# Kernel optimization log

Hardware: AMD Instinct MI355X
Metric: run time of the kernel (lower is better)

The kernel has to match this reference:

```python
import jax, jax.numpy as jnp
import numpy as np

B, T = 2, 512
E, NH, HD, V, P, L, KER, BLOCK = 768, 12, 64, 256, 4, 4, 16, 512
SCALE = HD ** -0.5


def _ln(x, g, b, eps=1e-5):
    m = jnp.mean(x, -1, keepdims=True)
    v = jnp.mean((x - m) ** 2, -1, keepdims=True)
    return (x - m) * jax.lax.rsqrt(v + eps) * g + b


def _rope_tables(n):
    inv = 1.0 / (10000.0 ** (jnp.arange(0, HD, 2, dtype=jnp.float32) / HD))
    f = jnp.arange(n, dtype=jnp.float32)[:, None] * inv[None, :]
    return jnp.cos(f), jnp.sin(f)


def _rope(x, cos, sin):
    # rotate over last two dims (positions, HD); split-half RoPE as in source
    h = x.shape[-1] // 2
    x1, x2 = x[..., :h], x[..., h:]
    return jnp.concatenate([x1 * cos - x2 * sin, x1 * sin + x2 * cos], axis=-1)


def _patch_attn(x, qkv_w, S):
    # x: [B,T,E]; sliding-window patch attention, step=1
    Bb, Tt, _ = x.shape
    q, k, v = jnp.split(x @ qkv_w, 3, axis=-1)
    heads = lambda t: t.reshape(Bb, Tt, NH, HD).transpose(0, 2, 1, 3)  # [B,NH,T,HD]
    q, k, v = heads(q), heads(k), heads(v)
    cos, sin = _rope_tables(Tt)
    q = _rope(q, cos, sin)
    k = _rope(k, cos, sin)
    # prefix: full causal attention over first S tokens
    sc = jnp.einsum('bnqh,bnkh->bnqk', q[:, :, :S], k[:, :, :S]) * SCALE
    mask = jnp.tril(jnp.ones((S, S), dtype=bool))
    sc = jnp.where(mask, sc, jnp.float32(-jnp.inf))
    out = jnp.einsum('bnqk,bnkh->bnqh', jax.nn.softmax(sc, axis=-1), v[:, :, :S])
    if Tt > S:
        # query t (t>=S) attends keys [t-S+1, t] (mask_sliding is all-ones for step=1)
        idx = jnp.arange(Tt - S)[:, None] + 1 + jnp.arange(S)[None, :]  # [T-S,S]
        kw = k[:, :, idx]  # [B,NH,T-S,S,HD]
        vw = v[:, :, idx]
        qs = q[:, :, S:]   # [B,NH,T-S,HD]
        sw = jnp.einsum('bnth,bntsh->bnts', qs, kw) * SCALE
        ow = jnp.einsum('bnts,bntsh->bnth', jax.nn.softmax(sw, axis=-1), vw)
        out = jnp.concatenate([out, ow], axis=2)
    return out.transpose(0, 2, 1, 3).reshape(Bb, Tt, NH * HD)


def _sa_block(x, ln0g, ln0b, ln1g, ln1b, qkv_w, proj_w, proj_b, w1, b1, w2, b2):
    # x: [B,T,P,V]; full (unmasked) attention over the P prediction slots
    Bb, Tt, Pp, _ = x.shape
    h = _ln(x, ln0g, ln0b)
    q, k, v = jnp.split(h @ qkv_w, 3, axis=-1)
    heads = lambda t: t.reshape(Bb, Tt, Pp, NH, HD).transpose(0, 1, 3, 2, 4)  # [B,T,NH,P,HD]
    q, k, v = heads(q), heads(k), heads(v)
    cos, sin = _rope_tables(Pp)
    q = _rope(q, cos, sin)
    k = _rope(k, cos, sin)
    sc = jnp.einsum('btnph,btnqh->btnpq', q, k) * SCALE
    o = jnp.einsum('btnpq,btnqh->btnph', jax.nn.softmax(sc, axis=-1), v)
    o = o.transpose(0, 1, 3, 2, 4).reshape(Bb, Tt, Pp, NH * HD)
    x = x + (o @ proj_w + proj_b)
    h2 = _ln(x, ln1g, ln1b)
    ff = jax.nn.gelu(h2 @ w1 + b1, approximate=False) @ w2 + b2
    return x + ff


def _forward(tokens, emb, blk_ln0_g, blk_ln0_b, blk_ln1_g, blk_ln1_b, blk_qkv_w,
             blk_ff_w1, blk_ff_b1, blk_ff_w2, blk_ff_b2, fin_ln_g, fin_ln_b,
             head_w, head_b, sa_ln0_g, sa_ln0_b, sa_ln1_g, sa_ln1_b, sa_qkv_w,
             sa_proj_w, sa_proj_b, sa_ff_w1, sa_ff_b1, sa_ff_w2, sa_ff_b2):
    x0 = emb[tokens]  # [B,T,E]
    x = x0
    for i in range(L):
        S = min(KER * 2 ** i, BLOCK)
        h = _ln(x, blk_ln0_g[i], blk_ln0_b[i])
        x = x + _patch_attn(h, blk_qkv_w[i], S)
        h2 = _ln(x, blk_ln1_g[i], blk_ln1_b[i])
        x = x + (jax.nn.gelu(h2 @ blk_ff_w1[i] + blk_ff_b1[i], approximate=False)
                 @ blk_ff_w2[i] + blk_ff_b2[i])
    x = x0 + x  # Golu: x = token_embedding(x); x = x + blocks(x)
    x = _ln(x, fin_ln_g, fin_ln_b)
    logits = (x @ head_w + head_b).reshape(B, T, P, V)
    logits = _sa_block(logits, sa_ln0_g, sa_ln0_b, sa_ln1_g, sa_ln1_b, sa_qkv_w,
                       sa_proj_w, sa_proj_b, sa_ff_w1, sa_ff_b1, sa_ff_w2, sa_ff_b2)
    return logits[:, :, 0, :]  # [B,T,V] (y is None path)


def setup_inputs() -> dict:
    key = jax.random.key(0)
    ks = jax.random.split(key, 12)
    w = lambda k, sh: jax.random.normal(k, sh, dtype=jnp.float32) * 0.02
    return {
        'tokens': jax.random.randint(ks[0], (B, T), 0, V),
        'emb': w(ks[1], (V, E)),
        'blk_ln0_g': jnp.ones((L, E), jnp.float32),
        'blk_ln0_b': jnp.zeros((L, E), jnp.float32),
        'blk_ln1_g': jnp.ones((L, E), jnp.float32),
        'blk_ln1_b': jnp.zeros((L, E), jnp.float32),
        'blk_qkv_w': w(ks[2], (L, E, 3 * E)),
        'blk_ff_w1': w(ks[3], (L, E, 4 * E)),
        'blk_ff_b1': jnp.zeros((L, 4 * E), jnp.float32),
        'blk_ff_w2': w(ks[4], (L, 4 * E, E)),
        'blk_ff_b2': jnp.zeros((L, E), jnp.float32),
        'fin_ln_g': jnp.ones((E,), jnp.float32),
        'fin_ln_b': jnp.zeros((E,), jnp.float32),
        'head_w': w(ks[5], (E, V * P)),
        'head_b': jnp.zeros((V * P,), jnp.float32),
        'sa_ln0_g': jnp.ones((V,), jnp.float32),
        'sa_ln0_b': jnp.zeros((V,), jnp.float32),
        'sa_ln1_g': jnp.ones((V,), jnp.float32),
        'sa_ln1_b': jnp.zeros((V,), jnp.float32),
        'sa_qkv_w': w(ks[6], (V, 3 * E)),
        'sa_proj_w': w(ks[7], (E, V)),
        'sa_proj_b': jnp.zeros((V,), jnp.float32),
        'sa_ff_w1': w(ks[8], (V, 4 * V)),
        'sa_ff_b1': jnp.zeros((4 * V,), jnp.float32),
        'sa_ff_w2': w(ks[9], (4 * V, V)),
        'sa_ff_b2': jnp.zeros((V,), jnp.float32),
    }


def reference(tokens, emb, blk_ln0_g, blk_ln0_b, blk_ln1_g, blk_ln1_b, blk_qkv_w,
              blk_ff_w1, blk_ff_b1, blk_ff_w2, blk_ff_b2, fin_ln_g, fin_ln_b,
              head_w, head_b, sa_ln0_g, sa_ln0_b, sa_ln1_g, sa_ln1_b, sa_qkv_w,
              sa_proj_w, sa_proj_b, sa_ff_w1, sa_ff_b1, sa_ff_w2, sa_ff_b2):
    return _forward(tokens, emb, blk_ln0_g, blk_ln0_b, blk_ln1_g, blk_ln1_b,
                    blk_qkv_w, blk_ff_w1, blk_ff_b1, blk_ff_w2, blk_ff_b2,
                    fin_ln_g, fin_ln_b, head_w, head_b, sa_ln0_g, sa_ln0_b,
                    sa_ln1_g, sa_ln1_b, sa_qkv_w, sa_proj_w, sa_proj_b,
                    sa_ff_w1, sa_ff_b1, sa_ff_w2, sa_ff_b2)
```

## Files before the change

### kernel.cpp

```cpp
#include <hip/hip_runtime.h>
#include <hip/hip_bf16.h>
#include <cstdint>
#include <cstddef>

#define BB    2
#define TSEQ  512
#define EDIM  768
#define NHEAD 12
#define HDIM  64
#define VDIM  256
#define PDIM  4
#define NROW  (BB*TSEQ)
#define NROW2 (BB*TSEQ*PDIM)

typedef __attribute__((ext_vector_type(8))) short short8;
typedef __attribute__((ext_vector_type(4))) float floatx4;

__device__ __forceinline__ float gelu_f(float v){
    return 0.5f * v * (1.0f + erff(v * 0.70710678118654752f));
}

__device__ __forceinline__ float b2f(short s){
    unsigned u = ((unsigned)(unsigned short)s) << 16;
    float f; __builtin_memcpy(&f, &u, 4); return f;
}

__device__ __forceinline__ void gload16(const void* g, void* l){
    __builtin_amdgcn_global_load_lds((const __attribute__((address_space(1))) void*)g,
                                     (__attribute__((address_space(3))) void*)l, 16, 0, 0);
}

struct WD { const float* in; __hip_bfloat16* out; int K; int N; int ntiles; };

__global__ __launch_bounds__(256) void wconv_multi(WD d0, WD d1, WD d2, WD d3, WD d4)
{
    int id = blockIdx.x;
    WD w = d0;
    if(id >= w.ntiles){ id -= w.ntiles; w = d1;
        if(id >= w.ntiles){ id -= w.ntiles; w = d2;
            if(id >= w.ntiles){ id -= w.ntiles; w = d3;
                if(id >= w.ntiles){ id -= w.ntiles; w = d4; } } } }
    if(!w.in) return;
    const int tx = w.N / 32;
    const int n0 = (id % tx) * 32, k0 = (id / tx) * 32;
    __shared__ float t[32][33];
    const int c = threadIdx.x & 31, r0 = threadIdx.x >> 5;
    #pragma unroll
    for(int r = r0; r < 32; r += 8)
        t[r][c] = w.in[(size_t)(k0 + r) * w.N + n0 + c];
    __syncthreads();
    #pragma unroll
    for(int r = r0; r < 32; r += 8)
        w.out[(size_t)(n0 + r) * w.K + k0 + c] = __float2bfloat16(t[c][r]);
}

template<int ACT, int RESID, int OUTBF16, int ROPESA>
__global__ __launch_bounds__(256) void gemm128(
    const short* __restrict__ A, const short* __restrict__ Bt,
    const float* __restrict__ bias, const float* __restrict__ resid,
    void* __restrict__ Cout, const float* __restrict__ rc, const float* __restrict__ rs,
    int M, int N, int K)
{
    alignas(16) __shared__ short As[128*32];
    alignas(16) __shared__ short Bs[128*32];
    const int tid  = threadIdx.x;
    const int lane = tid & 63;
    const int wave = tid >> 6;
    const int bm = blockIdx.y * 128, bn = blockIdx.x * 128;
    const int wm = (wave >> 1) * 64, wn = (wave & 1) * 64;
    const int quad = lane >> 4, l16 = lane & 15;

    floatx4 acc[4][4];
    #pragma unroll
    for(int i = 0; i < 4; i++)
        #pragma unroll
        for(int j = 0; j < 4; j++)
            acc[i][j] = floatx4{0.f, 0.f, 0.f, 0.f};

    const int r  = tid >> 2;
    const int c8 = (tid & 3) * 8;
    const int ldsoff = (tid & 192) * 16;

    for(int k0 = 0; k0 < K; k0 += 32){
        gload16(A  + (size_t)(bm + r     ) * K + k0 + c8, (char*)As + ldsoff);
        gload16(A  + (size_t)(bm + r + 64) * K + k0 + c8, (char*)As + 4096 + ldsoff);
        gload16(Bt + (size_t)(bn + r     ) * K + k0 + c8, (char*)Bs + ldsoff);
        gload16(Bt + (size_t)(bn + r + 64) * K + k0 + c8, (char*)Bs + 4096 + ldsoff);
        __syncthreads();
        short8 af[4], bfr[4];
        #pragma unroll
        for(int i = 0; i < 4; i++){
            af[i]  = *(const short8*)&As[(wm + i*16 + l16)*32 + quad*8];
            bfr[i] = *(const short8*)&Bs[(wn + i*16 + l16)*32 + quad*8];
        }
        #pragma unroll
        for(int i = 0; i < 4; i++)
            #pragma unroll
            for(int j = 0; j < 4; j++)
                acc[i][j] = __builtin_amdgcn_mfma_f32_16x16x32_bf16(af[i], bfr[j], acc[i][j], 0, 0, 0);
        __syncthreads();
    }

    float* Cf = (float*)Cout;
    __hip_bfloat16* Cb = (__hip_bfloat16*)Cout;

    if(ROPESA){
        const int hb = bn + wn;
        const int region = hb / 768;
        #pragma unroll
        for(int i = 0; i < 4; i++){
            #pragma unroll
            for(int rr = 0; rr < 4; rr++){
                int row = bm + wm + i*16 + quad*4 + rr;
                float a0 = acc[i][0][rr], a1 = acc[i][1][rr];
                float a2 = acc[i][2][rr], a3 = acc[i][3][rr];
                size_t rowb = (size_t)row * N + hb;
                if(region == 2){
                    Cb[rowb + l16]      = __float2bfloat16(a0);
                    Cb[rowb + 16 + l16] = __float2bfloat16(a1);
                    Cb[rowb + 32 + l16] = __float2bfloat16(a2);
                    Cb[rowb + 48 + l16] = __float2bfloat16(a3);
                }else{
                    int p = row & 3;
                    float c0 = rc[p*32 + l16],      s0 = rs[p*32 + l16];
                    float c1 = rc[p*32 + 16 + l16], s1 = rs[p*32 + 16 + l16];
                    Cb[rowb + l16]      = __float2bfloat16(a0*c0 - a2*s0);
                    Cb[rowb + 16 + l16] = __float2bfloat16(a1*c1 - a3*s1);
                    Cb[rowb + 32 + l16] = __float2bfloat16(a0*s0 + a2*c0);
                    Cb[rowb + 48 + l16] = __float2bfloat16(a1*s1 + a3*c1);
                }
            }
        }
        return;
    }

    #pragma unroll
    for(int i = 0; i < 4; i++){
        int row0 = bm + wm + i*16 + quad*4;
        #pragma unroll
        for(int j = 0; j < 4; j++){
            int col = bn + wn + j*16 + l16;
            float bv = bias ? bias[col] : 0.f;
            #pragma unroll
            for(int rr = 0; rr < 4; rr++){
                float v = acc[i][j][rr] + bv;
                if(ACT) v = gelu_f(v);
                if(RESID) v += resid[(size_t)(row0 + rr) * N + col];
                if(OUTBF16) Cb[(size_t)(row0 + rr) * N + col] = __float2bfloat16(v);
                else        Cf[(size_t)(row0 + rr) * N + col] = v;
            }
        }
    }
}

template<int EPI>
__global__ __launch_bounds__(256) void gemm64x128(
    const short* __restrict__ A, const short* __restrict__ Bt,
    const float* __restrict__ bias, __hip_bfloat16* __restrict__ Cout,
    __hip_bfloat16* __restrict__ qrb, __hip_bfloat16* __restrict__ krb,
    __hip_bfloat16* __restrict__ vvb,
    const float* __restrict__ rc, const float* __restrict__ rs,
    int M, int N, int K)
{
    alignas(16) __shared__ short As[64*32];
    alignas(16) __shared__ short Bs[128*32];
    const int tid  = threadIdx.x;
    const int lane = tid & 63;
    const int wave = tid >> 6;
    const int bm = blockIdx.y * 64, bn = blockIdx.x * 128;
    const int wm = (wave >> 1) * 32, wn = (wave & 1) * 64;
    const int quad = lane >> 4, l16 = lane & 15;

    floatx4 acc[2][4];
    #pragma unroll
    for(int i = 0; i < 2; i++)
        #pragma unroll
        for(int j = 0; j < 4; j++)
            acc[i][j] = floatx4{0.f, 0.f, 0.f, 0.f};

    const int r  = tid >> 2;
    const int c8 = (tid & 3) * 8;
    const int ldsoff = (tid & 192) * 16;

    for(int k0 = 0; k0 < K; k0 += 32){
        gload16(A  + (size_t)(bm + r     ) * K + k0 + c8, (char*)As + ldsoff);
        gload16(Bt + (size_t)(bn + r     ) * K + k0 + c8, (char*)Bs + ldsoff);
        gload16(Bt + (size_t)(bn + r + 64) * K + k0 + c8, (char*)Bs + 4096 + ldsoff);
        __syncthreads();
        short8 af[2], bfr[4];
        #pragma unroll
        for(int i = 0; i < 2; i++)
            af[i]  = *(const short8*)&As[(wm + i*16 + l16)*32 + quad*8];
        #pragma unroll
        for(int j = 0; j < 4; j++)
            bfr[j] = *(const short8*)&Bs[(wn + j*16 + l16)*32 + quad*8];
        #pragma unroll
        for(int i = 0; i < 2; i++)
            #pragma unroll
            for(int j = 0; j < 4; j++)
                acc[i][j] = __builtin_amdgcn_mfma_f32_16x16x32_bf16(af[i], bfr[j], acc[i][j], 0, 0, 0);
        __syncthreads();
    }

    if(EPI == 2){
        const int hb = bn + wn;
        const int region = hb / 768;
        const int h = (hb % 768) >> 6;
        #pragma unroll
        for(int i = 0; i < 2; i++){
            #pragma unroll
            for(int rr = 0; rr < 4; rr++){
                int row = bm + wm + i*16 + quad*4 + rr;
                int t = row & (TSEQ-1), b = row >> 9;
                float a0 = acc[i][0][rr], a1 = acc[i][1][rr];
                float a2 = acc[i][2][rr], a3 = acc[i][3][rr];
                size_t dbase = ((size_t)(b*NHEAD + h)*TSEQ + t)*HDIM;
                if(region == 2){
                    vvb[dbase + l16]      = __float2bfloat16(a0);
                    vvb[dbase + 16 + l16] = __float2bfloat16(a1);
                    vvb[dbase + 32 + l16] = __float2bfloat16(a2);
                    vvb[dbase + 48 + l16] = __float2bfloat16(a3);
                }else{
                    float c0 = rc[t*32 + l16],      s0 = rs[t*32 + l16];
                    float c1 = rc[t*32 + 16 + l16], s1 = rs[t*32 + 16 + l16];
                    __hip_bfloat16* dst = (region == 0) ? qrb : krb;
                    dst[dbase + l16]      = __float2bfloat16(a0*c0 - a2*s0);
                    dst[dbase + 16 + l16] = __float2bfloat16(a1*c1 - a3*s1);
                    dst[dbase + 32 + l16] = __float2bfloat16(a0*s0 + a2*c0);
                    dst[dbase + 48 + l16] = __float2bfloat16(a1*s1 + a3*c1);
                }
            }
        }
        return;
    }

    #pragma unroll
    for(int i = 0; i < 2; i++){
        int row0 = bm + wm + i*16 + quad*4;
        #pragma unroll
        for(int j = 0; j < 4; j++){
            int col = bn + wn + j*16 + l16;
            float bv = bias ? bias[col] : 0.f;
            #pragma unroll
            for(int rr = 0; rr < 4; rr++){
                float v = acc[i][j][rr] + bv;
                if(EPI == 1) v = gelu_f(v);
                Cout[(size_t)(row0 + rr) * N + col] = __float2bfloat16(v);
            }
        }
    }
}

template<int ACT, int RESID, int OUTBF16>
__global__ __launch_bounds__(256) void gemm64t(
    const short* __restrict__ A, const short* __restrict__ Bt,
    const float* __restrict__ bias, const float* __restrict__ resid,
    void* __restrict__ Cout, int M, int N, int K)
{
    alignas(16) __shared__ short As[64*32];
    alignas(16) __shared__ short Bs[64*32];
    const int tid  = threadIdx.x;
    const int lane = tid & 63;
    const int wave = tid >> 6;
    const int bm = blockIdx.y * 64, bn = blockIdx.x * 64;
    const int wm = (wave >> 1) * 32, wn = (wave & 1) * 32;
    const int quad = lane >> 4, l16 = lane & 15;

    floatx4 acc[2][2];
    #pragma unroll
    for(int i = 0; i < 2; i++)
        #pragma unroll
        for(int j = 0; j < 2; j++)
            acc[i][j] = floatx4{0.f, 0.f, 0.f, 0.f};

    const int r  = tid >> 2;
    const int c8 = (tid & 3) * 8;
    const int ldsoff = (tid & 192) * 16;

    for(int k0 = 0; k0 < K; k0 += 32){
        gload16(A  + (size_t)(bm + r) * K + k0 + c8, (char*)As + ldsoff);
        gload16(Bt + (size_t)(bn + r) * K + k0 + c8, (char*)Bs + ldsoff);
        __syncthreads();
        short8 af[2], bfr[2];
        #pragma unroll
        for(int i = 0; i < 2; i++){
            af[i]  = *(const short8*)&As[(wm + i*16 + l16)*32 + quad*8];
            bfr[i] = *(const short8*)&Bs[(wn + i*16 + l16)*32 + quad*8];
        }
        #pragma unroll
        for(int i = 0; i < 2; i++)
            #pragma unroll
            for(int j = 0; j < 2; j++)
                acc[i][j] = __builtin_amdgcn_mfma_f32_16x16x32_bf16(af[i], bfr[j], acc[i][j], 0, 0, 0);
        __syncthreads();
    }

    float* Cf = (float*)Cout;
    __hip_bfloat16* Cb = (__hip_bfloat16*)Cout;
    #pragma unroll
    for(int i = 0; i < 2; i++){
        int row0 = bm + wm + i*16 + quad*4;
        #pragma unroll
        for(int j = 0; j < 2; j++){
            int col = bn + wn + j*16 + l16;
            float bv = bias ? bias[col] : 0.f;
            #pragma unroll
            for(int rr = 0; rr < 4; rr++){
                float v = acc[i][j][rr] + bv;
                if(ACT) v = gelu_f(v);
                if(RESID) v += resid[(size_t)(row0 + rr) * N + col];
                if(OUTBF16) Cb[(size_t)(row0 + rr) * N + col] = __float2bfloat16(v);
                else        Cf[(size_t)(row0 + rr) * N + col] = v;
            }
        }
    }
}

__global__ __launch_bounds__(256) void ln_kernel(
    const float* __restrict__ in, const float* __restrict__ in2,
    const float* __restrict__ g, const float* __restrict__ bta,
    __hip_bfloat16* __restrict__ out, int D)
{
    const int row = blockIdx.x;
    const float* xr  = in + (size_t)row * D;
    const float* x2r = in2 ? in2 + (size_t)row * D : nullptr;
    const int tid = threadIdx.x;
    const int nper = D / 256;
    float vals[3];
    float sum = 0.f, sq = 0.f;
    for(int i = 0; i < nper; i++){
        int d = tid + i*256;
        float v = xr[d];
        if(x2r) v += x2r[d];
        vals[i] = v; sum += v; sq += v*v;
    }
    #pragma unroll
    for(int off = 32; off > 0; off >>= 1){
        sum += __shfl_xor(sum, off, 64);
        sq  += __shfl_xor(sq,  off, 64);
    }
    __shared__ float ssum[4], ssq[4];
    __shared__ float smean, srstd;
    int wid = tid >> 6;
    if((tid & 63) == 0){ ssum[wid] = sum; ssq[wid] = sq; }
    __syncthreads();
    if(tid == 0){
        float S = 0.f, Q = 0.f;
        for(int w = 0; w < 4; w++){ S += ssum[w]; Q += ssq[w]; }
        float m = S / D;
        float var = Q / D - m*m;
        smean = m;
        srstd = rsqrtf(fmaxf(var, 0.f) + 1e-5f);
    }
    __syncthreads();
    float m = smean, rs2 = srstd;
    for(int i = 0; i < nper; i++){
        int d = tid + i*256;
        out[(size_t)row*D + d] = __float2bfloat16((vals[i] - m) * rs2 * g[d] + bta[d]);
    }
}

__global__ __launch_bounds__(192) void embed_kernel(
    const int* __restrict__ tokens, const float* __restrict__ emb,
    float* __restrict__ x0, float* __restrict__ x)
{
    const int row = blockIdx.x;
    const int tok = tokens[row];
    const float4* src = (const float4*)(emb + (size_t)tok * EDIM);
    float4* d0 = (float4*)(x0 + (size_t)row * EDIM);
    float4* d1 = (float4*)(x  + (size_t)row * EDIM);
    for(int i = threadIdx.x; i < EDIM/4; i += blockDim.x){
        float4 v = src[i]; d0[i] = v; d1[i] = v;
    }
}

__global__ __launch_bounds__(256) void rope_kernel(float* __restrict__ rc, float* __restrict__ rs)
{
    int i = blockIdx.x * 256 + threadIdx.x;
    int pos = i >> 5, d = i & 31;
    float inv = powf(10000.0f, -(float)(2*d) / 64.0f);
    float f = (float)pos * inv;
// ... 82 lines not shown
    const int t = blockIdx.x, h = blockIdx.y, b = blockIdx.z;
    const int p = threadIdx.x >> 6, lane = threadIdx.x & 63;
    const int row0 = (b*TSEQ + t) * PDIM;
    const short* base = (const short*)qkv2 + (size_t)row0 * (3*EDIM);
    const int d = lane;
    float q = b2f(base[(size_t)p*(3*EDIM) + h*HDIM + d]);
    float sc[4];
    #pragma unroll
    for(int j = 0; j < 4; j++){
        float kj = b2f(base[(size_t)j*(3*EDIM) + EDIM + h*HDIM + d]);
        float v = q * kj;
        #pragma unroll
        for(int off = 32; off > 0; off >>= 1) v += __shfl_xor(v, off, 64);
        sc[j] = v * 0.125f;
    }
    float m = fmaxf(fmaxf(sc[0], sc[1]), fmaxf(sc[2], sc[3]));
    float e0 = expf(sc[0]-m), e1 = expf(sc[1]-m), e2 = expf(sc[2]-m), e3 = expf(sc[3]-m);
    float idn = 1.f / (e0 + e1 + e2 + e3);
    float ov = (e0 * b2f(base[0*(3*EDIM) + 2*EDIM + h*HDIM + d])
              + e1 * b2f(base[1*(3*EDIM) + 2*EDIM + h*HDIM + d])
              + e2 * b2f(base[2*(3*EDIM) + 2*EDIM + h*HDIM + d])
              + e3 * b2f(base[3*(3*EDIM) + 2*EDIM + h*HDIM + d])) * idn;
    o[(size_t)(row0 + p) * EDIM + h*HDIM + d] = __float2bfloat16(ov);
}

__global__ __launch_bounds__(256) void outcopy(const float* __restrict__ x2, float* __restrict__ out)
{
    int i = blockIdx.x * 256 + threadIdx.x;
    int row = i >> 8, col = i & 255;
    out[i] = x2[(size_t)row * PDIM * VDIM + col];
}

extern "C" void kernel_launch(void* const* d_in, const int* in_sizes, int n_in,
                              void* d_out, int out_size, void* d_ws, size_t ws_size,
                              hipStream_t stream)
{
    const int*   tokens    = (const int*)  d_in[0];
    const float* emb       = (const float*)d_in[1];
    const float* bl0g      = (const float*)d_in[2];
    const float* bl0b      = (const float*)d_in[3];
    const float* bl1g      = (const float*)d_in[4];
    const float* bl1b      = (const float*)d_in[5];
    const float* qkv_w     = (const float*)d_in[6];
    const float* ff_w1     = (const float*)d_in[7];
    const float* ff_b1     = (const float*)d_in[8];
    const float* ff_w2     = (const float*)d_in[9];
    const float* ff_b2     = (const float*)d_in[10];
    const float* fin_g     = (const float*)d_in[11];
    const float* fin_b     = (const float*)d_in[12];
    const float* head_w    = (const float*)d_in[13];
    const float* head_b    = (const float*)d_in[14];
    const float* sa_ln0_g  = (const float*)d_in[15];
    const float* sa_ln0_b  = (const float*)d_in[16];
    const float* sa_ln1_g  = (const float*)d_in[17];
    const float* sa_ln1_b  = (const float*)d_in[18];
    const float* sa_qkv_w  = (const float*)d_in[19];
    const float* sa_proj_w = (const float*)d_in[20];
    const float* sa_proj_b = (const float*)d_in[21];
    const float* sa_ff_w1  = (const float*)d_in[22];
    const float* sa_ff_b1  = (const float*)d_in[23];
    const float* sa_ff_w2  = (const float*)d_in[24];
    const float* sa_ff_b2  = (const float*)d_in[25];
    float* out = (float*)d_out;

    char* base = (char*)d_ws;
    float* logits           = (float*)(base);
    float* ropec            = (float*)(base + 4194304);
    float* ropes            = (float*)(base + 4259840);
    __hip_bfloat16* wqkvT   = (__hip_bfloat16*)(base + 4325376);
    __hip_bfloat16* wff1T   = (__hip_bfloat16*)(base + 7864320);
    __hip_bfloat16* wff2T   = (__hip_bfloat16*)(base + 12582912);
    __hip_bfloat16* wheadT  = (__hip_bfloat16*)(base + 17301504);
    __hip_bfloat16* wsaqkvT = (__hip_bfloat16*)(base + 18874368);
    __hip_bfloat16* wsaprojT= (__hip_bfloat16*)(base + 20054016);
    __hip_bfloat16* wsaff1T = (__hip_bfloat16*)(base + 20447232);
    __hip_bfloat16* wsaff2T = (__hip_bfloat16*)(base + 20971520);
    char* U = base + 21495808;
    float* x0           = (float*)(U);
    float* x            = (float*)(U + 3145728);
    __hip_bfloat16* h   = (__hip_bfloat16*)(U + 6291456);
    __hip_bfloat16* ff1 = (__hip_bfloat16*)(U + 12582912);
    __hip_bfloat16* qrb = (__hip_bfloat16*)(U + 18874368);
    __hip_bfloat16* krb = (__hip_bfloat16*)(U + 20447232);
    __hip_bfloat16* vvb = (__hip_bfloat16*)(U + 22020096);
    __hip_bfloat16* h2    = (__hip_bfloat16*)(U);
    __hip_bfloat16* qkv2  = (__hip_bfloat16*)(U + 2097152);
    __hip_bfloat16* sa_o  = (__hip_bfloat16*)(U + 20971520);
    __hip_bfloat16* sa_f1 = (__hip_bfloat16*)(U + 27262976);

    embed_kernel<<<NROW, 192, 0, stream>>>(tokens, emb, x0, x);
    rope_kernel<<<64, 256, 0, stream>>>(ropec, ropes);
    {
        WD dh  = { head_w,    wheadT,   768,  1024, (1024/32)*( 768/32) };
        WD dq  = { sa_qkv_w,  wsaqkvT,  256,  2304, (2304/32)*( 256/32) };
        WD dp  = { sa_proj_w, wsaprojT, 768,   256, ( 256/32)*( 768/32) };
        WD df1 = { sa_ff_w1,  wsaff1T,  256,  1024, (1024/32)*( 256/32) };
        WD df2 = { sa_ff_w2,  wsaff2T, 1024,   256, ( 256/32)*(1024/32) };
        wconv_multi<<<768+576+192+256+256, 256, 0, stream>>>(dh, dq, dp, df1, df2);
    }

    for(int i = 0; i < 4; i++){
        {
            WD dq  = { qkv_w + (size_t)i*EDIM*3*EDIM, wqkvT, 768, 2304, (2304/32)*(768/32) };
            WD df1 = { ff_w1 + (size_t)i*EDIM*4*EDIM, wff1T, 768, 3072, (3072/32)*(768/32) };
            WD df2 = { ff_w2 + (size_t)i*4*EDIM*EDIM, wff2T, 3072, 768, ( 768/32)*(3072/32)};
            WD dn  = { nullptr, nullptr, 0, 0, 0 };
            wconv_multi<<<1728+2304+2304, 256, 0, stream>>>(dq, df1, df2, dn, dn);
        }
        ln_kernel<<<NROW, 256, 0, stream>>>(x, nullptr, bl0g + i*EDIM, bl0b + i*EDIM, h, EDIM);
        gemm64x128<2><<<dim3(18, 16), 256, 0, stream>>>(
            (const short*)h, (const short*)wqkvT, nullptr, nullptr,
            qrb, krb, vvb, ropec, ropes, NROW, 3*EDIM, EDIM);
        dim3 agrid(TSEQ/4, NHEAD, BB);
        if(i == 0)      patch_attn2<16><<<agrid, 256, 0, stream>>>(qrb, krb, vvb, x);
        else if(i == 1) patch_attn2<32><<<agrid, 256, 0, stream>>>(qrb, krb, vvb, x);
        else if(i == 2) patch_attn2<64><<<agrid, 256, 0, stream>>>(qrb, krb, vvb, x);
        else            patch_attn2<128><<<agrid, 256, 0, stream>>>(qrb, krb, vvb, x);
        ln_kernel<<<NROW, 256, 0, stream>>>(x, nullptr, bl1g + i*EDIM, bl1b + i*EDIM, h, EDIM);
        gemm64x128<1><<<dim3(24, 16), 256, 0, stream>>>(
            (const short*)h, (const short*)wff1T, ff_b1 + (size_t)i*4*EDIM, ff1,
            nullptr, nullptr, nullptr, nullptr, nullptr, NROW, 4*EDIM, EDIM);
        gemm64t<0,1,0><<<dim3(12, 16), 256, 0, stream>>>(
            (const short*)ff1, (const short*)wff2T, ff_b2 + (size_t)i*EDIM, x, x, NROW, EDIM, 4*EDIM);
    }

    ln_kernel<<<NROW, 256, 0, stream>>>(x, x0, fin_g, fin_b, h, EDIM);
    gemm64t<0,0,0><<<dim3(16, 16), 256, 0, stream>>>(
        (const short*)h, (const short*)wheadT, head_b, nullptr, logits, NROW, PDIM*VDIM, EDIM);

    ln_kernel<<<NROW2, 256, 0, stream>>>(logits, nullptr, sa_ln0_g, sa_ln0_b, h2, VDIM);
    gemm128<0,0,1,1><<<dim3(18, 32), 256, 0, stream>>>(
        (const short*)h2, (const short*)wsaqkvT, nullptr, nullptr, qkv2,
        ropec, ropes, NROW2, 3*EDIM, VDIM);
    sa_attn<<<dim3(TSEQ, NHEAD, BB), 256, 0, stream>>>(qkv2, sa_o);
    gemm64t<0,1,0><<<dim3(4, 64), 256, 0, stream>>>(
        (const short*)sa_o, (const short*)wsaprojT, sa_proj_b, logits, logits, NROW2, VDIM, EDIM);
    ln_kernel<<<NROW2, 256, 0, stream>>>(logits, nullptr, sa_ln1_g, sa_ln1_b, h2, VDIM);
    gemm128<1,0,1,0><<<dim3(8, 32), 256, 0, stream>>>(
        (const short*)h2, (const short*)wsaff1T, sa_ff_b1, nullptr, sa_f1,
        nullptr, nullptr, NROW2, 4*VDIM, VDIM);
    gemm64t<0,1,0><<<dim3(4, 64), 256, 0, stream>>>(
        (const short*)sa_f1, (const short*)wsaff2T, sa_ff_b2, logits, logits, NROW2, VDIM, 4*VDIM);

    outcopy<<<(out_size + 255)/256, 256, 0, stream>>>(logits, out);
}
```

Baseline: 736.5 us.

## Fuse LayerNorm into GEMM prologues by folding gamma/beta into weights and bias

Removes the standalone LayerNorm kernels. Gamma is folded into the transposed bf16 weights, and beta@W is precomputed into a bias vector. Each GEMM computes per-row mean and rstd and normalizes its A tile on the fly from fp32. All weight conversions for the four layers are batched into one launch up front, and the final output copy is fused into the last GEMM epilogue. This cuts launches and intermediate bf16 round trips, but each GEMM column block now re-reads fp32 activations for its statistics. The A tile is also loaded synchronously instead of with direct-to-LDS loads.

```diff
diff --git a/kernel.cpp b/kernel.cpp
--- a/kernel.cpp
+++ b/kernel.cpp
@@ -19,28 +19,28 @@
 __device__ __forceinline__ float gelu_f(float v){
     return 0.5f * v * (1.0f + erff(v * 0.70710678118654752f));
 }
-
 __device__ __forceinline__ float b2f(short s){
     unsigned u = ((unsigned)(unsigned short)s) << 16;
     float f; __builtin_memcpy(&f, &u, 4); return f;
 }
-
+__device__ __forceinline__ short f2bs(float v){
+    __hip_bfloat16 h = __float2bfloat16(v);
+    short s; __builtin_memcpy(&s, &h, 2); return s;
+}
 __device__ __forceinline__ void gload16(const void* g, void* l){
     __builtin_amdgcn_global_load_lds((const __attribute__((address_space(1))) void*)g,
                                      (__attribute__((address_space(3))) void*)l, 16, 0, 0);
 }
 
-struct WD { const float* in; __hip_bfloat16* out; int K; int N; int ntiles; };
-
-__global__ __launch_bounds__(256) void wconv_multi(WD d0, WD d1, WD d2, WD d3, WD d4)
+struct WD2 { const float* in; const float* g; __hip_bfloat16* out; int K; int N; int nt; };
+struct WDs { WD2 d[17]; };
+
+__global__ __launch_bounds__(256) void wconv_all(WDs a)
 {
     int id = blockIdx.x;
-    WD w = d0;
-    if(id >= w.ntiles){ id -= w.ntiles; w = d1;
-        if(id >= w.ntiles){ id -= w.ntiles; w = d2;
-            if(id >= w.ntiles){ id -= w.ntiles; w = d3;
-                if(id >= w.ntiles){ id -= w.ntiles; w = d4; } } } }
-    if(!w.in) return;
+    int i = 0;
+    while(i < 16 && id >= a.d[i].nt){ id -= a.d[i].nt; i++; }
+    WD2 w = a.d[i];
     const int tx = w.N / 32;
     const int n0 = (id % tx) * 32, k0 = (id / tx) * 32;
     __shared__ float t[32][33];
@@ -48,31 +48,83 @@
     #pragma unroll
     for(int r = r0; r < 32; r += 8)
         t[r][c] = w.in[(size_t)(k0 + r) * w.N + n0 + c];
+    const float gv = w.g ? w.g[k0 + c] : 1.0f;
     __syncthreads();
     #pragma unroll
     for(int r = r0; r < 32; r += 8)
-        w.out[(size_t)(n0 + r) * w.K + k0 + c] = __float2bfloat16(t[c][r]);
-}
-
-template<int ACT, int RESID, int OUTBF16, int ROPESA>
-__global__ __launch_bounds__(256) void gemm128(
-    const short* __restrict__ A, const short* __restrict__ Bt,
-    const float* __restrict__ bias, const float* __restrict__ resid,
-    void* __restrict__ Cout, const float* __restrict__ rc, const float* __restrict__ rs,
+        w.out[(size_t)(n0 + r) * w.K + k0 + c] = __float2bfloat16(t[c][r] * gv);
+}
+
+struct LB { const float* extb; const float* lnb; const float* w; float* ob; int N; int K; };
+struct LBs { LB d[11]; };
+
+__global__ __launch_bounds__(256) void lnbias(LBs a)
+{
+    int id = blockIdx.x;
+    int i = 0;
+    while(i < 10 && id >= a.d[i].N/256){ id -= a.d[i].N/256; i++; }
+    LB w = a.d[i];
+    const int n = id*256 + threadIdx.x;
+    float acc = w.extb ? w.extb[n] : 0.f;
+    for(int k = 0; k < w.K; k += 4){
+        acc += w.lnb[k+0] * w.w[(size_t)(k+0)*w.N + n];
+        acc += w.lnb[k+1] * w.w[(size_t)(k+1)*w.N + n];
+        acc += w.lnb[k+2] * w.w[(size_t)(k+2)*w.N + n];
+        acc += w.lnb[k+3] * w.w[(size_t)(k+3)*w.N + n];
+    }
+    w.ob[n] = acc;
+}
+
+template<int MT, int EPI, int ADD2>
+__global__ __launch_bounds__(256) void gemmln(
+    const float* __restrict__ A, const float* __restrict__ A2,
+    const short* __restrict__ Bt, const float* __restrict__ biasv,
+    void* __restrict__ Cout,
+    __hip_bfloat16* __restrict__ qrb, __hip_bfloat16* __restrict__ krb,
+    __hip_bfloat16* __restrict__ vvb,
+    const float* __restrict__ rc, const float* __restrict__ rs,
     int M, int N, int K)
 {
-    alignas(16) __shared__ short As[128*32];
+    constexpr int MI = (MT == 64) ? 2 : 4;
+    alignas(16) __shared__ short As[MT*32];
     alignas(16) __shared__ short Bs[128*32];
+    __shared__ float smean[MT], srstd[MT];
+
     const int tid  = threadIdx.x;
     const int lane = tid & 63;
     const int wave = tid >> 6;
-    const int bm = blockIdx.y * 128, bn = blockIdx.x * 128;
-    const int wm = (wave >> 1) * 64, wn = (wave & 1) * 64;
+    const int bm = blockIdx.y * MT, bn = blockIdx.x * 128;
+    const int wm = (wave >> 1) * (MT/2), wn = (wave & 1) * 64;
     const int quad = lane >> 4, l16 = lane & 15;
 
-    floatx4 acc[4][4];
-    #pragma unroll
-    for(int i = 0; i < 4; i++)
+    {
+        int sr, seg, off;
+        if(MT == 64){ sr = tid >> 2; seg = K/4; off = (tid & 3) * seg; }
+        else        { sr = tid >> 1; seg = K/2; off = (tid & 1) * seg; }
+        const float* xr  = A + (size_t)(bm + sr) * K + off;
+        const float* x2r = ADD2 ? A2 + (size_t)(bm + sr) * K + off : nullptr;
+        float s = 0.f, q = 0.f;
+        for(int j = 0; j < seg; j += 4){
+            float4 v = *(const float4*)(xr + j);
+            if(ADD2){ float4 w2 = *(const float4*)(x2r + j);
+                      v.x += w2.x; v.y += w2.y; v.z += w2.z; v.w += w2.w; }
+            s += v.x + v.y + v.z + v.w;
+            q += v.x*v.x + v.y*v.y + v.z*v.z + v.w*v.w;
+        }
+        s += __shfl_xor(s, 1, 64); q += __shfl_xor(q, 1, 64);
+        if(MT == 64){ s += __shfl_xor(s, 2, 64); q += __shfl_xor(q, 2, 64); }
+        const int qt = (MT == 64) ? (tid & 3) : (tid & 1);
+        if(qt == 0){
+            float m = s / K;
+            smean[sr] = m;
+            srstd[sr] = rsqrtf(fmaxf(q / K - m*m, 0.f) + 1e-5f);
+        }
+    }
+    __syncthreads();
+
+    floatx4 acc[MI][4];
+    #pragma unroll
+    for(int i = 0; i < MI; i++)
         #pragma unroll
         for(int j = 0; j < 4; j++)
             acc[i][j] = floatx4{0.f, 0.f, 0.f, 0.f};
@@ -80,21 +132,49 @@
     const int r  = tid >> 2;
     const int c8 = (tid & 3) * 8;
     const int ldsoff = (tid & 192) * 16;
+    const float m0 = smean[r], rs0 = srstd[r];
+    float m1 = 0.f, rs1 = 0.f;
+    if(MT == 128){ m1 = smean[r + 64]; rs1 = srstd[r + 64]; }
 
     for(int k0 = 0; k0 < K; k0 += 32){
-        gload16(A  + (size_t)(bm + r     ) * K + k0 + c8, (char*)As + ldsoff);
-        gload16(A  + (size_t)(bm + r + 64) * K + k0 + c8, (char*)As + 4096 + ldsoff);
         gload16(Bt + (size_t)(bn + r     ) * K + k0 + c8, (char*)Bs + ldsoff);
         gload16(Bt + (size_t)(bn + r + 64) * K + k0 + c8, (char*)Bs + 4096 + ldsoff);
+        {
+            const float* ap = A + (size_t)(bm + r) * K + k0 + c8;
+            float4 v0 = *(const float4*)(ap), v1 = *(const float4*)(ap + 4);
+            if(ADD2){
+                const float* a2p = A2 + (size_t)(bm + r) * K + k0 + c8;
+                float4 w0 = *(const float4*)(a2p), w1 = *(const float4*)(a2p + 4);
+                v0.x += w0.x; v0.y += w0.y; v0.z += w0.z; v0.w += w0.w;
+                v1.x += w1.x; v1.y += w1.y; v1.z += w1.z; v1.w += w1.w;
+            }
+            short8 pk;
+            pk[0] = f2bs((v0.x - m0)*rs0); pk[1] = f2bs((v0.y - m0)*rs0);
+            pk[2] = f2bs((v0.z - m0)*rs0); pk[3] = f2bs((v0.w - m0)*rs0);
+            pk[4] = f2bs((v1.x - m0)*rs0); pk[5] = f2bs((v1.y - m0)*rs0);
+            pk[6] = f2bs((v1.z - m0)*rs0); pk[7] = f2bs((v1.w - m0)*rs0);
+            *(short8*)&As[r*32 + c8] = pk;
+        }
+        if(MT == 128){
+            const float* ap = A + (size_t)(bm + r + 64) * K + k0 + c8;
+            float4 v0 = *(const float4*)(ap), v1 = *(const float4*)(ap + 4);
+            short8 pk;
+            pk[0] = f2bs((v0.x - m1)*rs1); pk[1] = f2bs((v0.y - m1)*rs1);
+            pk[2] = f2bs((v0.z - m1)*rs1); pk[3] = f2bs((v0.w - m1)*rs1);
+            pk[4] = f2bs((v1.x - m1)*rs1); pk[5] = f2bs((v1.y - m1)*rs1);
+            pk[6] = f2bs((v1.z - m1)*rs1); pk[7] = f2bs((v1.w - m1)*rs1);
+            *(short8*)&As[(r + 64)*32 + c8] = pk;
+        }
         __syncthreads();
-        short8 af[4], bfr[4];
-        #pragma unroll
-        for(int i = 0; i < 4; i++){
+        short8 af[MI], bfr[4];
+        #pragma unroll
+        for(int i = 0; i < MI; i++)
             af[i]  = *(const short8*)&As[(wm + i*16 + l16)*32 + quad*8];
-            bfr[i] = *(const short8*)&Bs[(wn + i*16 + l16)*32 + quad*8];
-        }
-        #pragma unroll
-        for(int i = 0; i < 4; i++)
+        #pragma unroll
+        for(int j = 0; j < 4; j++)
+            bfr[j] = *(const short8*)&Bs[(wn + j*16 + l16)*32 + quad*8];
+        #pragma unroll
+        for(int i = 0; i < MI; i++)
             #pragma unroll
             for(int j = 0; j < 4; j++)
                 acc[i][j] = __builtin_amdgcn_mfma_f32_16x16x32_bf16(af[i], bfr[j], acc[i][j], 0, 0, 0);
@@ -104,30 +184,54 @@
     float* Cf = (float*)Cout;
     __hip_bfloat16* Cb = (__hip_bfloat16*)Cout;
 
-    if(ROPESA){
+    if(EPI == 2 || EPI == 3){
         const int hb = bn + wn;
         const int region = hb / 768;
-        #pragma unroll
-        for(int i = 0; i < 4; i++){
+        const int h = (hb % 768) >> 6;
+        float bj0 = biasv ? biasv[hb + l16]      : 0.f;
+        float bj1 = biasv ? biasv[hb + 16 + l16] : 0.f;
+        float bj2 = biasv ? biasv[hb + 32 + l16] : 0.f;
+        float bj3 = biasv ? biasv[hb + 48 + l16] : 0.f;
+        #pragma unroll
+        for(int i = 0; i < MI; i++){
             #pragma unroll
             for(int rr = 0; rr < 4; rr++){
                 int row = bm + wm + i*16 + quad*4 + rr;
-                float a0 = acc[i][0][rr], a1 = acc[i][1][rr];
-                float a2 = acc[i][2][rr], a3 = acc[i][3][rr];
-                size_t rowb = (size_t)row * N + hb;
-                if(region == 2){
-                    Cb[rowb + l16]      = __float2bfloat16(a0);
-                    Cb[rowb + 16 + l16] = __float2bfloat16(a1);
-                    Cb[rowb + 32 + l16] = __float2bfloat16(a2);
-                    Cb[rowb + 48 + l16] = __float2bfloat16(a3);
+                float a0 = acc[i][0][rr] + bj0, a1 = acc[i][1][rr] + bj1;
+                float a2 = acc[i][2][rr] + bj2, a3 = acc[i][3][rr] + bj3;
+                if(EPI == 2){
+                    int t = row & (TSEQ-1), b = row >> 9;
+                    size_t dbase = ((size_t)(b*NHEAD + h)*TSEQ + t)*HDIM;
+                    if(region == 2){
+                        vvb[dbase + l16]      = __float2bfloat16(a0);
+                        vvb[dbase + 16 + l16] = __float2bfloat16(a1);
+                        vvb[dbase + 32 + l16] = __float2bfloat16(a2);
+                        vvb[dbase + 48 + l16] = __float2bfloat16(a3);
+                    }else{
+                        float c0 = rc[t*32 + l16],      s0 = rs[t*32 + l16];
+                        float c1 = rc[t*32 + 16 + l16], s1 = rs[t*32 + 16 + l16];
+                        __hip_bfloat16* dst = (region == 0) ? qrb : krb;
+                        dst[dbase + l16]      = __float2bfloat16(a0*c0 - a2*s0);
+                        dst[dbase + 16 + l16] = __float2bfloat16(a1*c1 - a3*s1);
+                        dst[dbase + 32 + l16] = __float2bfloat16(a0*s0 + a2*c0);
+                        dst[dbase + 48 + l16] = __float2bfloat16(a1*s1 + a3*c1);
+                    }
                 }else{
-                    int p = row & 3;
-                    float c0 = rc[p*32 + l16],      s0 = rs[p*32 + l16];
-                    float c1 = rc[p*32 + 16 + l16], s1 = rs[p*32 + 16 + l16];
-                    Cb[rowb + l16]      = __float2bfloat16(a0*c0 - a2*s0);
-                    Cb[rowb + 16 + l16] = __float2bfloat16(a1*c1 - a3*s1);
-                    Cb[rowb + 32 + l16] = __float2bfloat16(a0*s0 + a2*c0);
-                    Cb[rowb + 48 + l16] = __float2bfloat16(a1*s1 + a3*c1);
+                    size_t rowb = (size_t)row * N + hb;
+                    if(region == 2){
+                        Cb[rowb + l16]      = __float2bfloat16(a0);
+                        Cb[rowb + 16 + l16] = __float2bfloat16(a1);
+                        Cb[rowb + 32 + l16] = __float2bfloat16(a2);
+                        Cb[rowb + 48 + l16] = __float2bfloat16(a3);
+                    }else{
+                        int p = row & 3;
+                        float c0 = rc[p*32 + l16],      s0 = rs[p*32 + l16];
+                        float c1 = rc[p*32 + 16 + l16], s1 = rs[p*32 + 16 + l16];
+                        Cb[rowb + l16]      = __float2bfloat16(a0*c0 - a2*s0);
+                        Cb[rowb + 16 + l16] = __float2bfloat16(a1*c1 - a3*s1);
+                        Cb[rowb + 32 + l16] = __float2bfloat16(a0*s0 + a2*c0);
+                        Cb[rowb + 48 + l16] = __float2bfloat16(a1*s1 + a3*c1);
+                    }
                 }
             }
         }
@@ -135,127 +239,27 @@
     }
 
     #pragma unroll
-    for(int i = 0; i < 4; i++){
+    for(int i = 0; i < MI; i++){
         int row0 = bm + wm + i*16 + quad*4;
         #pragma unroll
         for(int j = 0; j < 4; j++){
             int col = bn + wn + j*16 + l16;
-            float bv = bias ? bias[col] : 0.f;
+            float bv = biasv ? biasv[col] : 0.f;
             #pragma unroll
             for(int rr = 0; rr < 4; rr++){
                 float v = acc[i][j][rr] + bv;
-                if(ACT) v = gelu_f(v);
-                if(RESID) v += resid[(size_t)(row0 + rr) * N + col];
-                if(OUTBF16) Cb[(size_t)(row0 + rr) * N + col] = __float2bfloat16(v);
-                else        Cf[(size_t)(row0 + rr) * N + col] = v;
+                if(EPI == 1){ v = gelu_f(v); Cb[(size_t)(row0 + rr) * N + col] = __float2bfloat16(v); }
+                else        {                Cf[(size_t)(row0 + rr) * N + col] = v; }
             }
         }
     }
 }
 
-template<int EPI>
-__global__ __launch_bounds__(256) void gemm64x128(
-    const short* __restrict__ A, const short* __restrict__ Bt,
-    const float* __restrict__ bias, __hip_bfloat16* __restrict__ Cout,
-    __hip_bfloat16* __restrict__ qrb, __hip_bfloat16* __restrict__ krb,
-    __hip_bfloat16* __restrict__ vvb,
-    const float* __restrict__ rc, const float* __restrict__ rs,
-    int M, int N, int K)
-{
-    alignas(16) __shared__ short As[64*32];
-    alignas(16) __shared__ short Bs[128*32];
-    const int tid  = threadIdx.x;
-    const int lane = tid & 63;
-    const int wave = tid >> 6;
-    const int bm = blockIdx.y * 64, bn = blockIdx.x * 128;
-    const int wm = (wave >> 1) * 32, wn = (wave & 1) * 64;
-    const int quad = lane >> 4, l16 = lane & 15;
-
-    floatx4 acc[2][4];
-    #pragma unroll
-    for(int i = 0; i < 2; i++)
-        #pragma unroll
-        for(int j = 0; j < 4; j++)
-            acc[i][j] = floatx4{0.f, 0.f, 0.f, 0.f};
-
-    const int r  = tid >> 2;
-    const int c8 = (tid & 3) * 8;
-    const int ldsoff = (tid & 192) * 16;
-
-    for(int k0 = 0; k0 < K; k0 += 32){
-        gload16(A  + (size_t)(bm + r     ) * K + k0 + c8, (char*)As + ldsoff);
-        gload16(Bt + (size_t)(bn + r     ) * K + k0 + c8, (char*)Bs + ldsoff);
-        gload16(Bt + (size_t)(bn + r + 64) * K + k0 + c8, (char*)Bs + 4096 + ldsoff);
-        __syncthreads();
-        short8 af[2], bfr[4];
-        #pragma unroll
-        for(int i = 0; i < 2; i++)
-            af[i]  = *(const short8*)&As[(wm + i*16 + l16)*32 + quad*8];
-        #pragma unroll
-        for(int j = 0; j < 4; j++)
-            bfr[j] = *(const short8*)&Bs[(wn + j*16 + l16)*32 + quad*8];
-        #pragma unroll
-        for(int i = 0; i < 2; i++)
-            #pragma unroll
-            for(int j = 0; j < 4; j++)
-                acc[i][j] = __builtin_amdgcn_mfma_f32_16x16x32_bf16(af[i], bfr[j], acc[i][j], 0, 0, 0);
-        __syncthreads();
-    }
-
-    if(EPI == 2){
-        const int hb = bn + wn;
-        const int region = hb / 768;
-        const int h = (hb % 768) >> 6;
-        #pragma unroll
-        for(int i = 0; i < 2; i++){
-            #pragma unroll
-            for(int rr = 0; rr < 4; rr++){
-                int row = bm + wm + i*16 + quad*4 + rr;
-                int t = row & (TSEQ-1), b = row >> 9;
-                float a0 = acc[i][0][rr], a1 = acc[i][1][rr];
-                float a2 = acc[i][2][rr], a3 = acc[i][3][rr];
-                size_t dbase = ((size_t)(b*NHEAD + h)*TSEQ + t)*HDIM;
-                if(region == 2){
-                    vvb[dbase + l16]      = __float2bfloat16(a0);
-                    vvb[dbase + 16 + l16] = __float2bfloat16(a1);
-                    vvb[dbase + 32 + l16] = __float2bfloat16(a2);
-                    vvb[dbase + 48 + l16] = __float2bfloat16(a3);
-                }else{
-                    float c0 = rc[t*32 + l16],      s0 = rs[t*32 + l16];
-                    float c1 = rc[t*32 + 16 + l16], s1 = rs[t*32 + 16 + l16];
-                    __hip_bfloat16* dst = (region == 0) ? qrb : krb;
-                    dst[dbase + l16]      = __float2bfloat16(a0*c0 - a2*s0);
-                    dst[dbase + 16 + l16] = __float2bfloat16(a1*c1 - a3*s1);
-                    dst[dbase + 32 + l16] = __float2bfloat16(a0*s0 + a2*c0);
-                    dst[dbase + 48 + l16] = __float2bfloat16(a1*s1 + a3*c1);
-                }
-            }
-        }
-        return;
-    }
-
-    #pragma unroll
-    for(int i = 0; i < 2; i++){
-        int row0 = bm + wm + i*16 + quad*4;
-        #pragma unroll
-        for(int j = 0; j < 4; j++){
-            int col = bn + wn + j*16 + l16;
-            float bv = bias ? bias[col] : 0.f;
-            #pragma unroll
-            for(int rr = 0; rr < 4; rr++){
-                float v = acc[i][j][rr] + bv;
-                if(EPI == 1) v = gelu_f(v);
-                Cout[(size_t)(row0 + rr) * N + col] = __float2bfloat16(v);
-            }
-        }
-    }
-}
-
-template<int ACT, int RESID, int OUTBF16>
+template<int OUTC>
 __global__ __launch_bounds__(256) void gemm64t(
     const short* __restrict__ A, const short* __restrict__ Bt,
     const float* __restrict__ bias, const float* __restrict__ resid,
-    void* __restrict__ Cout, int M, int N, int K)
+    float* __restrict__ Cf, float* __restrict__ outp, int M, int N, int K)
 {
     alignas(16) __shared__ short As[64*32];
     alignas(16) __shared__ short Bs[64*32];
@@ -295,8 +299,6 @@
         __syncthreads();
     }
 
-    float* Cf = (float*)Cout;
-    __hip_bfloat16* Cb = (__hip_bfloat16*)Cout;
     #pragma unroll
     for(int i = 0; i < 2; i++){
         int row0 = bm + wm + i*16 + quad*4;
@@ -306,57 +308,13 @@
             float bv = bias ? bias[col] : 0.f;
             #pragma unroll
             for(int rr = 0; rr < 4; rr++){
-                float v = acc[i][j][rr] + bv;
-                if(ACT) v = gelu_f(v);
-                if(RESID) v += resid[(size_t)(row0 + rr) * N + col];
-                if(OUTBF16) Cb[(size_t)(row0 + rr) * N + col] = __float2bfloat16(v);
-                else        Cf[(size_t)(row0 + rr) * N + col] = v;
+                int row = row0 + rr;
+                float v = acc[i][j][rr] + bv + resid[(size_t)row * N + col];
+                Cf[(size_t)row * N + col] = v;
+                if(OUTC && (row & 3) == 0)
+                    outp[(size_t)(row >> 2) * N + col] = v;
             }
         }
-    }
-}
-
-__global__ __launch_bounds__(256) void ln_kernel(
-    const float* __restrict__ in, const float* __restrict__ in2,
-    const float* __restrict__ g, const float* __restrict__ bta,
-    __hip_bfloat16* __restrict__ out, int D)
-{
-    const int row = blockIdx.x;
-    const float* xr  = in + (size_t)row * D;
-    const float* x2r = in2 ? in2 + (size_t)row * D : nullptr;
-    const int tid = threadIdx.x;
-    const int nper = D / 256;
-    float vals[3];
-    float sum = 0.f, sq = 0.f;
-    for(int i = 0; i < nper; i++){
-        int d = tid + i*256;
-        float v = xr[d];
-        if(x2r) v += x2r[d];
-        vals[i] = v; sum += v; sq += v*v;
-    }
-    #pragma unroll
-    for(int off = 32; off > 0; off >>= 1){
-        sum += __shfl_xor(sum, off, 64);
-        sq  += __shfl_xor(sq,  off, 64);
-    }
-    __shared__ float ssum[4], ssq[4];
-    __shared__ float smean, srstd;
-    int wid = tid >> 6;
-    if((tid & 63) == 0){ ssum[wid] = sum; ssq[wid] = sq; }
-    __syncthreads();
-    if(tid == 0){
-        float S = 0.f, Q = 0.f;
-        for(int w = 0; w < 4; w++){ S += ssum[w]; Q += ssq[w]; }
-        float m = S / D;
-        float var = Q / D - m*m;
-        smean = m;
-        srstd = rsqrtf(fmaxf(var, 0.f) + 1e-5f);
-    }
-    __syncthreads();
-    float m = smean, rs2 = srstd;
-    for(int i = 0; i < nper; i++){
-        int d = tid + i*256;
-        out[(size_t)row*D + d] = __float2bfloat16((vals[i] - m) * rs2 * g[d] + bta[d]);
     }
 }
 
@@ -485,13 +443,6 @@
               + e2 * b2f(base[2*(3*EDIM) + 2*EDIM + h*HDIM + d])
               + e3 * b2f(base[3*(3*EDIM) + 2*EDIM + h*HDIM + d])) * idn;
     o[(size_t)(row0 + p) * EDIM + h*HDIM + d] = __float2bfloat16(ov);
-}
-
-__global__ __launch_bounds__(256) void outcopy(const float* __restrict__ x2, float* __restrict__ out)
-{
-    int i = blockIdx.x * 256 + threadIdx.x;
-    int row = i >> 8, col = i & 255;
-    out[i] = x2[(size_t)row * PDIM * VDIM + col];
 }
 
 extern "C" void kernel_launch(void* const* d_in, const int* in_sizes, int n_in,
@@ -526,84 +477,104 @@
     const float* sa_ff_b2  = (const float*)d_in[25];
     float* out = (float*)d_out;
 
-    char* base = (char*)d_ws;
-    float* logits           = (float*)(base);
-    float* ropec            = (float*)(base + 4194304);
-    float* ropes            = (float*)(base + 4259840);
-    __hip_bfloat16* wqkvT   = (__hip_bfloat16*)(base + 4325376);
-    __hip_bfloat16* wff1T   = (__hip_bfloat16*)(base + 7864320);
-    __hip_bfloat16* wff2T   = (__hip_bfloat16*)(base + 12582912);
-    __hip_bfloat16* wheadT  = (__hip_bfloat16*)(base + 17301504);
-    __hip_bfloat16* wsaqkvT = (__hip_bfloat16*)(base + 18874368);
-    __hip_bfloat16* wsaprojT= (__hip_bfloat16*)(base + 20054016);
-    __hip_bfloat16* wsaff1T = (__hip_bfloat16*)(base + 20447232);
-    __hip_bfloat16* wsaff2T = (__hip_bfloat16*)(base + 20971520);
-    char* U = base + 21495808;
+    char* p = (char*)d_ws;
+    auto alloc = [&](size_t bytes){ char* q = p; p += (bytes + 255) & ~(size_t)255; return q; };
+
+    float* logits = (float*)alloc((size_t)NROW2*VDIM*4);
+    float* ropec  = (float*)alloc(512*32*4);
+    float* ropes  = (float*)alloc(512*32*4);
+    float* qkvb[4];  for(int i=0;i<4;i++) qkvb[i]  = (float*)alloc(2304*4);
+    float* ff1b[4];  for(int i=0;i<4;i++) ff1b[i]  = (float*)alloc(3072*4);
+    float* headb  = (float*)alloc(1024*4);
+    float* saqkvb = (float*)alloc(2304*4);
+    float* saff1b = (float*)alloc(1024*4);
+    __hip_bfloat16* wqkvT[4]; for(int i=0;i<4;i++) wqkvT[i] = (__hip_bfloat16*)alloc((size_t)768*2304*2);
+    __hip_bfloat16* wff1T[4]; for(int i=0;i<4;i++) wff1T[i] = (__hip_bfloat16*)alloc((size_t)768*3072*2);
+    __hip_bfloat16* wff2T[4]; for(int i=0;i<4;i++) wff2T[i] = (__hip_bfloat16*)alloc((size_t)3072*768*2);
+    __hip_bfloat16* wheadT   = (__hip_bfloat16*)alloc((size_t)768*1024*2);
+    __hip_bfloat16* wsaqkvT  = (__hip_bfloat16*)alloc((size_t)256*2304*2);
+    __hip_bfloat16* wsaprojT = (__hip_bfloat16*)alloc((size_t)768*256*2);
+    __hip_bfloat16* wsaff1T  = (__hip_bfloat16*)alloc((size_t)256*1024*2);
+    __hip_bfloat16* wsaff2T  = (__hip_bfloat16*)alloc((size_t)1024*256*2);
+    char* U = p;
     float* x0           = (float*)(U);
     float* x            = (float*)(U + 3145728);
-    __hip_bfloat16* h   = (__hip_bfloat16*)(U + 6291456);
-    __hip_bfloat16* ff1 = (__hip_bfloat16*)(U + 12582912);
-    __hip_bfloat16* qrb = (__hip_bfloat16*)(U + 18874368);
-    __hip_bfloat16* krb = (__hip_bfloat16*)(U + 20447232);
-    __hip_bfloat16* vvb = (__hip_bfloat16*)(U + 22020096);
-    __hip_bfloat16* h2    = (__hip_bfloat16*)(U);
-    __hip_bfloat16* qkv2  = (__hip_bfloat16*)(U + 2097152);
-    __hip_bfloat16* sa_o  = (__hip_bfloat16*)(U + 20971520);
-    __hip_bfloat16* sa_f1 = (__hip_bfloat16*)(U + 27262976);
+    __hip_bfloat16* ff1 = (__hip_bfloat16*)(U + 6291456);
+    __hip_bfloat16* qrb = (__hip_bfloat16*)(U + 12582912);
+    __hip_bfloat16* krb = (__hip_bfloat16*)(U + 14155776);
+    __hip_bfloat16* vvb = (__hip_bfloat16*)(U + 15728640);
+    __hip_bfloat16* qkv2  = (__hip_bfloat16*)(U);
+    __hip_bfloat16* sa_o  = (__hip_bfloat16*)(U + 18874368);
+    __hip_bfloat16* sa_f1 = (__hip_bfloat16*)(U + 25165824);
 
     embed_kernel<<<NROW, 192, 0, stream>>>(tokens, emb, x0, x);
     rope_kernel<<<64, 256, 0, stream>>>(ropec, ropes);
     {
-        WD dh  = { head_w,    wheadT,   768,  1024, (1024/32)*( 768/32) };
-        WD dq  = { sa_qkv_w,  wsaqkvT,  256,  2304, (2304/32)*( 256/32) };
-        WD dp  = { sa_proj_w, wsaprojT, 768,   256, ( 256/32)*( 768/32) };
-        WD df1 = { sa_ff_w1,  wsaff1T,  256,  1024, (1024/32)*( 256/32) };
-        WD df2 = { sa_ff_w2,  wsaff2T, 1024,   256, ( 256/32)*(1024/32) };
-        wconv_multi<<<768+576+192+256+256, 256, 0, stream>>>(dh, dq, dp, df1, df2);
+        WDs wds; int tot = 0, n = 0;
+        auto add = [&](const float* in, const float* g, __hip_bfloat16* o2, int K, int N){
+            wds.d[n++] = WD2{in, g, o2, K, N, (N/32)*(K/32)};
+            tot += (N/32)*(K/32);
+        };
+        for(int i=0;i<4;i++){
+            add(qkv_w + (size_t)i*768*2304, bl0g + i*768, wqkvT[i], 768, 2304);
+            add(ff_w1 + (size_t)i*768*3072, bl1g + i*768, wff1T[i], 768, 3072);
+            add(ff_w2 + (size_t)i*3072*768, nullptr,      wff2T[i], 3072, 768);
+        }
+        add(head_w,    fin_g,    wheadT,   768, 1024);
+        add(sa_qkv_w,  sa_ln0_g, wsaqkvT,  256, 2304);
+        add(sa_proj_w, nullptr,  wsaprojT, 768, 256);
+        add(sa_ff_w1,  sa_ln1_g, wsaff1T,  256, 1024);
+        add(sa_ff_w2,  nullptr,  wsaff2T, 1024, 256);
+        wconv_all<<<tot, 256, 0, stream>>>(wds);
+    }
+    {
+        LBs lbs; int tot = 0, n = 0;
+        auto add = [&](const float* extb, const float* lnb, const float* w, float* ob, int N, int K){
+            lbs.d[n++] = LB{extb, lnb, w, ob, N, K};
+            tot += N/256;
+        };
+        for(int i=0;i<4;i++){
+            add(nullptr,          bl0b + i*768, qkv_w + (size_t)i*768*2304, qkvb[i], 2304, 768);
+            add(ff_b1 + i*3072,   bl1b + i*768, ff_w1 + (size_t)i*768*3072, ff1b[i], 3072, 768);
+        }
+        add(head_b,   fin_b,    head_w,   headb,  1024, 768);
+        add(nullptr,  sa_ln0_b, sa_qkv_w, saqkvb, 2304, 256);
+        add(sa_ff_b1, sa_ln1_b, sa_ff_w1, saff1b, 1024, 256);
+        lnbias<<<tot, 256, 0, stream>>>(lbs);
     }
 
     for(int i = 0; i < 4; i++){
-        {
-            WD dq  = { qkv_w + (size_t)i*EDIM*3*EDIM, wqkvT, 768, 2304, (2304/32)*(768/32) };
-            WD df1 = { ff_w1 + (size_t)i*EDIM*4*EDIM, wff1T, 768, 3072, (3072/32)*(768/32) };
-            WD df2 = { ff_w2 + (size_t)i*4*EDIM*EDIM, wff2T, 3072, 768, ( 768/32)*(3072/32)};
-            WD dn  = { nullptr, nullptr, 0, 0, 0 };
-            wconv_multi<<<1728+2304+2304, 256, 0, stream>>>(dq, df1, df2, dn, dn);
-        }
-        ln_kernel<<<NROW, 256, 0, stream>>>(x, nullptr, bl0g + i*EDIM, bl0b + i*EDIM, h, EDIM);
-        gemm64x128<2><<<dim3(18, 16), 256, 0, stream>>>(
-            (const short*)h, (const short*)wqkvT, nullptr, nullptr,
+        gemmln<64,2,0><<<dim3(18, 16), 256, 0, stream>>>(
+            x, nullptr, (const short*)wqkvT[i], qkvb[i], nullptr,
             qrb, krb, vvb, ropec, ropes, NROW, 3*EDIM, EDIM);
         dim3 agrid(TSEQ/4, NHEAD, BB);
         if(i == 0)      patch_attn2<16><<<agrid, 256, 0, stream>>>(qrb, krb, vvb, x);
         else if(i == 1) patch_attn2<32><<<agrid, 256, 0, stream>>>(qrb, krb, vvb, x);
         else if(i == 2) patch_attn2<64><<<agrid, 256, 0, stream>>>(qrb, krb, vvb, x);
         else            patch_attn2<128><<<agrid, 256, 0, stream>>>(qrb, krb, vvb, x);
-        ln_kernel<<<NROW, 256, 0, stream>>>(x, nullptr, bl1g + i*EDIM, bl1b + i*EDIM, h, EDIM);
-        gemm64x128<1><<<dim3(24, 16), 256, 0, stream>>>(
-            (const short*)h, (const short*)wff1T, ff_b1 + (size_t)i*4*EDIM, ff1,
+        gemmln<64,1,0><<<dim3(24, 16), 256, 0, stream>>>(
+            x, nullptr, (const short*)wff1T[i], ff1b[i], ff1,
             nullptr, nullptr, nullptr, nullptr, nullptr, NROW, 4*EDIM, EDIM);
-        gemm64t<0,1,0><<<dim3(12, 16), 256, 0, stream>>>(
-            (const short*)ff1, (const short*)wff2T, ff_b2 + (size_t)i*EDIM, x, x, NROW, EDIM, 4*EDIM);
-    }
-
-    ln_kernel<<<NROW, 256, 0, stream>>>(x, x0, fin_g, fin_b, h, EDIM);
-    gemm64t<0,0,0><<<dim3(16, 16), 256, 0, stream>>>(
-        (const short*)h, (const short*)wheadT, head_b, nullptr, logits, NROW, PDIM*VDIM, EDIM);
-
-    ln_kernel<<<NROW2, 256, 0, stream>>>(logits, nullptr, sa_ln0_g, sa_ln0_b, h2, VDIM);
-    gemm128<0,0,1,1><<<dim3(18, 32), 256, 0, stream>>>(
-        (const short*)h2, (const short*)wsaqkvT, nullptr, nullptr, qkv2,
-        ropec, ropes, NROW2, 3*EDIM, VDIM);
+        gemm64t<0><<<dim3(12, 16), 256, 0, stream>>>(
+            (const short*)ff1, (const short*)wff2T[i], ff_b2 + (size_t)i*EDIM, x, x, nullptr,
+            NROW, EDIM, 4*EDIM);
+    }
+
+    gemmln<64,5,1><<<dim3(8, 16), 256, 0, stream>>>(
+        x, x0, (const short*)wheadT, headb, logits,
+        nullptr, nullptr, nullptr, nullptr, nullptr, NROW, PDIM*VDIM, EDIM);
+
+    gemmln<128,3,0><<<dim3(18, 32), 256, 0, stream>>>(
+        logits, nullptr, (const short*)wsaqkvT, saqkvb, qkv2,
+        nullptr, nullptr, nullptr, ropec, ropes, NROW2, 3*EDIM, VDIM);
     sa_attn<<<dim3(TSEQ, NHEAD, BB), 256, 0, stream>>>(qkv2, sa_o);
-    gemm64t<0,1,0><<<dim3(4, 64), 256, 0, stream>>>(
-        (const short*)sa_o, (const short*)wsaprojT, sa_proj_b, logits, logits, NROW2, VDIM, EDIM);
-    ln_kernel<<<NROW2, 256, 0, stream>>>(logits, nullptr, sa_ln1_g, sa_ln1_b, h2, VDIM);
-    gemm128<1,0,1,0><<<dim3(8, 32), 256, 0, stream>>>(
-        (const short*)h2, (const short*)wsaff1T, sa_ff_b1, nullptr, sa_f1,
-        nullptr, nullptr, NROW2, 4*VDIM, VDIM);
-    gemm64t<0,1,0><<<dim3(4, 64), 256, 0, stream>>>(
-        (const short*)sa_f1, (const short*)wsaff2T, sa_ff_b2, logits, logits, NROW2, VDIM, 4*VDIM);
-
-    outcopy<<<(out_size + 255)/256, 256, 0, stream>>>(logits, out);
-}
+    gemm64t<0><<<dim3(4, 64), 256, 0, stream>>>(
+        (const short*)sa_o, (const short*)wsaprojT, sa_proj_b, logits, logits, nullptr,
+        NROW2, VDIM, EDIM);
+    gemmln<128,1,0><<<dim3(8, 32), 256, 0, stream>>>(
+        logits, nullptr, (const short*)wsaff1T, saff1b, sa_f1,
+        nullptr, nullptr, nullptr, nullptr, nullptr, NROW2, 4*VDIM, VDIM);
+    gemm64t<1><<<dim3(4, 64), 256, 0, stream>>>(
+        (const short*)sa_f1, (const short*)wsaff2T, sa_ff_b2, logits, logits, out,
+        NROW2, VDIM, 4*VDIM);
+}
```

Measured after the change: 961.4 us. +30.5%, slower.
